# Kernel tuning notes

Measured on AMD Instinct MI355X. Metric: run time of the kernel, lower is better.

## Reference

```python
import jax, jax.numpy as jnp
import numpy as np

N = 100000   # num_nodes
E = 1000000  # num_edges
H = 64       # h_dim
OUT = 16     # out_dim (num classes)
R = 90       # num_rels
B = 8        # num_bases


def setup_inputs() -> dict:
    key = jax.random.key(0)
    ks = jax.random.split(key, 16)
    feats = jax.random.normal(ks[0], (N, H), dtype=jnp.float32)
    src = jax.random.randint(ks[1], (E,), 0, N)
    dst = jax.random.randint(ks[2], (E,), 0, N)
    etype = jax.random.randint(ks[3], (E,), 0, R)
    norm = jax.random.uniform(ks[4], (E, 1), dtype=jnp.float32)
    s_in = 1.0 / np.sqrt(H)
    s_b = 1.0 / np.sqrt(B)
    # layer 0: H->H, layer 1 (hidden): H->H, layer 2: H->OUT
    coeff0 = jax.random.normal(ks[5], (R, B), dtype=jnp.float32) * s_b
    bases0 = jax.random.normal(ks[6], (B, H, H), dtype=jnp.float32) * s_in
    bias0 = jnp.zeros((H,), dtype=jnp.float32)
    coeff1 = jax.random.normal(ks[7], (R, B), dtype=jnp.float32) * s_b
    bases1 = jax.random.normal(ks[8], (B, H, H), dtype=jnp.float32) * s_in
    bias1 = jnp.zeros((H,), dtype=jnp.float32)
    coeff2 = jax.random.normal(ks[9], (R, B), dtype=jnp.float32) * s_b
    bases2 = jax.random.normal(ks[10], (B, H, OUT), dtype=jnp.float32) * s_in
    bias2 = jnp.zeros((OUT,), dtype=jnp.float32)
    return {
        "feats": feats,
        "coeff0": coeff0, "bases0": bases0, "bias0": bias0,
        "coeff1": coeff1, "bases1": bases1, "bias1": bias1,
        "coeff2": coeff2, "bases2": bases2, "bias2": bias2,
        "src": src, "dst": dst, "etype": etype, "norm": norm,
    }


def _rgcn_layer(x, coeff, bases, bias, src, dst, etype, norm, relu):
    # Basis decomposition: W_r = sum_b coeff[r,b] * bases[b]
    # Project all nodes through every basis once: [N, B, out]
    Hn = jnp.einsum('ni,bio->nbo', x, bases)
    c = coeff[etype]  # [E, B] per-edge basis coefficients
    # Per-edge message m_e = (sum_b c_eb * Hn[src_e, b]) * norm_e,
    # accumulated over the (small, fixed) basis dim to avoid an [E,B,out] buffer.
    m = c[:, 0:1] * Hn[src, 0]
    for b in range(1, bases.shape[0]):
        m = m + c[:, b:b + 1] * Hn[src, b]
    m = m * norm
    h = jax.ops.segment_sum(m, dst, num_segments=x.shape[0]) + bias
    return jax.nn.relu(h) if relu else h


def reference(feats, coeff0, bases0, bias0, coeff1, bases1, bias1,
              coeff2, bases2, bias2, src, dst, etype, norm):
    h = _rgcn_layer(feats, coeff0, bases0, bias0, src, dst, etype, norm, relu=True)
    h = _rgcn_layer(h, coeff1, bases1, bias1, src, dst, etype, norm, relu=True)
    h = _rgcn_layer(h, coeff2, bases2, bias2, src, dst, etype, norm, relu=False)
    return h
```

## Files before the change

### kernel.cpp

```cpp
#include <hip/hip_runtime.h>
#include <hip/hip_bf16.h>
#include <cstdint>

#define NNODES 100000
#define NEDGES 1000000
#define HDIM 64
#define ODIM 16
#define NB 8
#define NREL 90
#define KDIM (HDIM * NB)

typedef short short8 __attribute__((ext_vector_type(8)));
typedef float f32x4  __attribute__((ext_vector_type(4)));
union FragU { uint4 u; short8 s; };

__device__ __forceinline__ float asf(uint32_t u) { float f; __builtin_memcpy(&f, &u, 4); return f; }
__device__ __forceinline__ uint32_t asu(float f) { uint32_t u; __builtin_memcpy(&u, &f, 4); return u; }
__device__ __forceinline__ uint16_t f2bf(float f) {
    uint32_t x = asu(f);
    return (uint16_t)((x + 0x7FFFu + ((x >> 16) & 1u)) >> 16);
}
__device__ __forceinline__ uint32_t pack2(float lo, float hi) {
    return (uint32_t)f2bf(lo) | ((uint32_t)f2bf(hi) << 16);
}
__device__ __forceinline__ void fmaC(const float4& cA, const float4& cB, float xs,
                                     float* __restrict__ acc) {
    acc[0] = fmaf(cA.x, xs, acc[0]); acc[1] = fmaf(cA.y, xs, acc[1]);
    acc[2] = fmaf(cA.z, xs, acc[2]); acc[3] = fmaf(cA.w, xs, acc[3]);
    acc[4] = fmaf(cB.x, xs, acc[4]); acc[5] = fmaf(cB.y, xs, acc[5]);
    acc[6] = fmaf(cB.z, xs, acc[6]); acc[7] = fmaf(cB.w, xs, acc[7]);
}

__global__ void cast_kernel(const float* __restrict__ in, uint16_t* __restrict__ out, int n4) {
    const int stride = (int)(gridDim.x * blockDim.x);
    for (int idx = (int)(blockIdx.x * blockDim.x + threadIdx.x); idx < n4; idx += stride) {
        float4 v = reinterpret_cast<const float4*>(in)[idx];
        uint2 p;
        p.x = pack2(v.x, v.y);
        p.y = pack2(v.z, v.w);
        reinterpret_cast<uint2*>(out)[idx] = p;
    }
}

__global__ void zero_kernel(int* __restrict__ p, int n) {
    for (int i = (int)(blockIdx.x * blockDim.x + threadIdx.x); i < n;
         i += (int)(gridDim.x * blockDim.x)) p[i] = 0;
}

__global__ void hist_kernel(const int* __restrict__ dst, int* __restrict__ cnt, int nE) {
    for (int e = (int)(blockIdx.x * blockDim.x + threadIdx.x); e < nE;
         e += (int)(gridDim.x * blockDim.x)) atomicAdd(&cnt[dst[e]], 1);
}

#define SCAN_B 512
__launch_bounds__(SCAN_B)
__global__ void scan_partial_kernel(const int* __restrict__ cnt, int* __restrict__ bsum, int n) {
    __shared__ int sh[SCAN_B];
    int id = (int)(blockIdx.x * SCAN_B + threadIdx.x);
    sh[threadIdx.x] = (id < n) ? cnt[id] : 0;
    __syncthreads();
    for (int off = SCAN_B / 2; off > 0; off >>= 1) {
        if ((int)threadIdx.x < off) sh[threadIdx.x] += sh[threadIdx.x + off];
        __syncthreads();
    }
    if (threadIdx.x == 0) bsum[blockIdx.x] = sh[0];
}

__launch_bounds__(256)
__global__ void scan_base_kernel(const int* __restrict__ bsum, int* __restrict__ bbase,
                                 int* __restrict__ offs, int nblk, int nNodes) {
    __shared__ int sh[256];
    const int t = (int)threadIdx.x;
    int v = (t < nblk) ? bsum[t] : 0;
    sh[t] = v;
    __syncthreads();
    for (int off = 1; off < 256; off <<= 1) {
        int tmp = (t >= off) ? sh[t - off] : 0;
        __syncthreads();
        sh[t] += tmp;
        __syncthreads();
    }
    if (t < nblk) bbase[t] = sh[t] - v;
    if (t == 255) offs[nNodes] = sh[255];
}

__launch_bounds__(SCAN_B)
__global__ void scan_final_kernel(int* __restrict__ cnt, const int* __restrict__ bbase,
                                  int* __restrict__ offs, int n) {
    __shared__ int sh[SCAN_B];
    int id = (int)(blockIdx.x * SCAN_B + threadIdx.x);
    int v = (id < n) ? cnt[id] : 0;
    sh[threadIdx.x] = v;
    __syncthreads();
    for (int off = 1; off < SCAN_B; off <<= 1) {
        int tmp = ((int)threadIdx.x >= off) ? sh[threadIdx.x - off] : 0;
        __syncthreads();
        sh[threadIdx.x] += tmp;
        __syncthreads();
    }
    if (id < n) {
        int excl = sh[threadIdx.x] - v + bbase[blockIdx.x];
        offs[id] = excl;
        cnt[id]  = excl;
    }
}

__global__ void scatter_kernel(const int* __restrict__ src, const int* __restrict__ dst,
                               const int* __restrict__ et, const float* __restrict__ norm,
                               int* __restrict__ cursor, uint2* __restrict__ rec, int nE) {
    const int tid    = (int)(blockIdx.x * blockDim.x + threadIdx.x);
    const int stride = (int)(gridDim.x * blockDim.x);
    int e = tid * 4;
    for (; e + 4 <= nE; e += stride * 4) {
        const int4   d4 = *reinterpret_cast<const int4*>(dst + e);
        const int4   s4 = *reinterpret_cast<const int4*>(src + e);
        const int4   t4 = *reinterpret_cast<const int4*>(et + e);
        const float4 n4 = *reinterpret_cast<const float4*>(norm + e);
        const int p0 = atomicAdd(&cursor[d4.x], 1);
        const int p1 = atomicAdd(&cursor[d4.y], 1);
        const int p2 = atomicAdd(&cursor[d4.z], 1);
        const int p3 = atomicAdd(&cursor[d4.w], 1);
        rec[p0] = make_uint2((uint32_t)s4.x | ((uint32_t)t4.x << 20), asu(n4.x));
        rec[p1] = make_uint2((uint32_t)s4.y | ((uint32_t)t4.y << 20), asu(n4.y));
        rec[p2] = make_uint2((uint32_t)s4.z | ((uint32_t)t4.z << 20), asu(n4.z));
        rec[p3] = make_uint2((uint32_t)s4.w | ((uint32_t)t4.w << 20), asu(n4.w));
    }
    for (; e < nE; e++) {
        int p = atomicAdd(&cursor[dst[e]], 1);
        rec[p] = make_uint2((uint32_t)src[e] | ((uint32_t)et[e] << 20), asu(norm[e]));
    }
}

__launch_bounds__(256)
__global__ void csr_agg_kernel(const uint16_t* __restrict__ x,
                               const float* __restrict__ coeff,
                               const int* __restrict__ offs,
                               const uint2* __restrict__ rec,
                               uint16_t* __restrict__ G, int nNodes) {
    __shared__ __align__(16) float cS[NREL * NB];
    for (int i = (int)threadIdx.x; i < NREL * NB; i += 256) cS[i] = coeff[i];
    __syncthreads();

    const int hl   = (int)threadIdx.x & 31;
    const int hwid = (int)((blockIdx.x * blockDim.x + threadIdx.x) >> 5);
    const int nhw  = (int)((gridDim.x * blockDim.x) >> 5);

    for (int d = hwid; d < nNodes; d += nhw) {
        const int j0 = offs[d], j1 = offs[d + 1];
        float accL[NB] = {0.f, 0.f, 0.f, 0.f, 0.f, 0.f, 0.f, 0.f};
        float accH[NB] = {0.f, 0.f, 0.f, 0.f, 0.f, 0.f, 0.f, 0.f};
        int j = j0;
        for (; j + 8 <= j1; j += 8) {
            uint2 r[8];
#pragma unroll
            for (int u = 0; u < 8; u++) r[u] = rec[j + u];
            uint32_t w[8];
#pragma unroll
            for (int u = 0; u < 8; u++)
                w[u] = *reinterpret_cast<const uint32_t*>(
                    x + (size_t)(r[u].x & 0xFFFFFu) * HDIM + 2 * hl);
#pragma unroll
            for (int u = 0; u < 8; u++) {
                const float4 cA = *reinterpret_cast<const float4*>(cS + (r[u].x >> 20) * NB);
                const float4 cB = *reinterpret_cast<const float4*>(cS + (r[u].x >> 20) * NB + 4);
                const float nm = asf(r[u].y);
                fmaC(cA, cB, asf(w[u] << 16) * nm, accL);
                fmaC(cA, cB, asf(w[u] & 0xFFFF0000u) * nm, accH);
            }
        }
        for (; j < j1; j++) {
            const uint2 r0 = rec[j];
            const uint32_t w0 = *reinterpret_cast<const uint32_t*>(
                x + (size_t)(r0.x & 0xFFFFFu) * HDIM + 2 * hl);
            const float4 cA = *reinterpret_cast<const float4*>(cS + (r0.x >> 20) * NB);
            const float4 cB = *reinterpret_cast<const float4*>(cS + (r0.x >> 20) * NB + 4);
            const float nm = asf(r0.y);
            fmaC(cA, cB, asf(w0 << 16) * nm, accL);
            fmaC(cA, cB, asf(w0 & 0xFFFF0000u) * nm, accH);
        }
        uint4 lo, hi;
        lo.x = pack2(accL[0], accL[1]); lo.y = pack2(accL[2], accL[3]);
        lo.z = pack2(accL[4], accL[5]); lo.w = pack2(accL[6], accL[7]);
        hi.x = pack2(accH[0], accH[1]); hi.y = pack2(accH[2], accH[3]);
        hi.z = pack2(accH[4], accH[5]); hi.w = pack2(accH[6], accH[7]);
        uint16_t* gp = G + (size_t)d * KDIM + hl * 16;
        *reinterpret_cast<uint4*>(gp)     = lo;
        *reinterpret_cast<uint4*>(gp + 8) = hi;
    }
}

__launch_bounds__(256, 3)
__global__ void proj_hidden_kernel(const uint16_t* __restrict__ G,
                                   const float* __restrict__ bases,
                                   const float* __restrict__ bias,
                                   uint16_t* __restrict__ xout, int nNodes) {
    const int t    = (int)threadIdx.x;
    const int lane = t & 63;
    const int ot   = t >> 6;
    const int q    = lane >> 4;
    const int c    = lane & 15;

    FragU bf[16];
#pragma unroll
    for (int kb = 0; kb < 16; kb++) {
#pragma unroll
        for (int j = 0; j < 8; j++) {
            const int k = kb * 32 + q * 8 + j;
            const int i = k >> 3, b = k & 7;
            bf[kb].s[j] = (short)f2bf(bases[(size_t)(b * HDIM + i) * HDIM + ot * 16 + c]);
        }
    }
    const float bv = bias[ot * 16 + c];

    const int nTiles = (nNodes + 63) / 64;
    for (int tile = (int)blockIdx.x; tile < nTiles; tile += (int)gridDim.x) {
#pragma unroll
        for (int g = 0; g < 4; g++) {
            int arow = tile * 64 + g * 16 + c;
            if (arow > nNodes - 1) arow = nNodes - 1;
            const uint16_t* gp = G + (size_t)arow * KDIM + q * 8;

            f32x4 acc = {0.f, 0.f, 0.f, 0.f};
#pragma unroll
            for (int kb = 0; kb < 16; kb++) {
                FragU a;
                a.u = *reinterpret_cast<const uint4*>(gp + kb * 32);
                acc = __builtin_amdgcn_mfma_f32_16x16x32_bf16(a.s, bf[kb].s, acc, 0, 0, 0);
            }

            const int nbase = tile * 64 + g * 16 + q * 4;
#pragma unroll
            for (int r = 0; r < 4; r++) {
                const int node = nbase + r;
                if (node < nNodes) {
                    float v = fmaxf(acc[r] + bv, 0.f);
                    xout[(size_t)node * HDIM + ot * 16 + c] = f2bf(v);
                }
            }
        }
    }
}

__launch_bounds__(256, 3)
__global__ void proj_out_kernel(const uint16_t* __restrict__ G,
                                const float* __restrict__ bases,
                                const float* __restrict__ bias,
                                float* __restrict__ out, int nNodes) {
    const int t    = (int)threadIdx.x;
    const int lane = t & 63;
    const int w    = t >> 6;
    const int q    = lane >> 4;
    const int c    = lane & 15;

    FragU bf[16];
#pragma unroll
    for (int kb = 0; kb < 16; kb++) {
#pragma unroll
        for (int j = 0; j < 8; j++) {
            const int k = kb * 32 + q * 8 + j;
            const int i = k >> 3, b = k & 7;
            bf[kb].s[j] = (short)f2bf(bases[(size_t)(b * HDIM + i) * ODIM + c]);
        }
    }
    const float bv = bias[c];

    const int nTiles = (nNodes + 63) / 64;
    for (int tile = (int)blockIdx.x; tile < nTiles; tile += (int)gridDim.x) {
        int arow = tile * 64 + w * 16 + c;
        if (arow > nNodes - 1) arow = nNodes - 1;
        const uint16_t* gp = G + (size_t)arow * KDIM + q * 8;

        f32x4 acc = {0.f, 0.f, 0.f, 0.f};
#pragma unroll
        for (int kb = 0; kb < 16; kb++) {
            FragU a;
            a.u = *reinterpret_cast<const uint4*>(gp + kb * 32);
            acc = __builtin_amdgcn_mfma_f32_16x16x32_bf16(a.s, bf[kb].s, acc, 0, 0, 0);
        }

        const int nbase = tile * 64 + w * 16 + q * 4;
#pragma unroll
        for (int r = 0; r < 4; r++) {
            const int node = nbase + r;
            if (node < nNodes) out[(size_t)node * ODIM + c] = acc[r] + bv;
        }
    }
}

extern "C" void kernel_launch(void* const* d_in, const int* in_sizes, int n_in,
                              void* d_out, int out_size, void* d_ws, size_t ws_size,
                              hipStream_t stream) {
    const float* feats  = (const float*)d_in[0];
    const float* coeff0 = (const float*)d_in[1];
    const float* bases0 = (const float*)d_in[2];
    const float* bias0  = (const float*)d_in[3];
    const float* coeff1 = (const float*)d_in[4];
    const float* bases1 = (const float*)d_in[5];
    const float* bias1  = (const float*)d_in[6];
    const float* coeff2 = (const float*)d_in[7];
    const float* bases2 = (const float*)d_in[8];
    const float* bias2  = (const float*)d_in[9];
    const int*   src    = (const int*)d_in[10];
    const int*   dst    = (const int*)d_in[11];
    const int*   etype  = (const int*)d_in[12];
    const float* norm   = (const float*)d_in[13];
    float* out = (float*)d_out;

    char* base = (char*)d_ws;
    uint16_t* G = (uint16_t*)base;
    uint16_t* x = (uint16_t*)(base + (size_t)NNODES * KDIM * 2);
    const size_t OFF_OFFS  = 115200000;
    const size_t OFF_CURS  = OFF_OFFS + 400016;
    const size_t OFF_BSUM  = OFF_CURS + 400016;
    const size_t OFF_BBASE = OFF_BSUM + 1024;
    const size_t OFF_REC   = OFF_BBASE + 1024;
    int*   offs  = (int*)(base + OFF_OFFS);
    int*   curs  = (int*)(base + OFF_CURS);
    int*   bsum  = (int*)(base + OFF_BSUM);
    int*   bbase = (int*)(base + OFF_BBASE);
    uint2* rec   = (uint2*)(base + OFF_REC);

    const int nblk = (NNODES + SCAN_B - 1) / SCAN_B;

    hipLaunchKernelGGL(zero_kernel, dim3(256), dim3(256), 0, stream, curs, NNODES);
    hipLaunchKernelGGL(hist_kernel, dim3(2048), dim3(256), 0, stream, dst, curs, NEDGES);
    hipLaunchKernelGGL(scan_partial_kernel, dim3(nblk), dim3(SCAN_B), 0, stream, curs, bsum, NNODES);
    hipLaunchKernelGGL(scan_base_kernel, dim3(1), dim3(256), 0, stream, bsum, bbase, offs, nblk, NNODES);
    hipLaunchKernelGGL(scan_final_kernel, dim3(nblk), dim3(SCAN_B), 0, stream, curs, bbase, offs, NNODES);
    hipLaunchKernelGGL(scatter_kernel, dim3(1024), dim3(256), 0, stream,
                       src, dst, etype, norm, curs, rec, NEDGES);

    hipLaunchKernelGGL(cast_kernel, dim3(2048), dim3(256), 0, stream,
                       feats, x, NNODES * HDIM / 4);

    hipLaunchKernelGGL(csr_agg_kernel, dim3(2048), dim3(256), 0, stream,
                       x, coeff0, offs, rec, G, NNODES);
    hipLaunchKernelGGL(proj_hidden_kernel, dim3(1024), dim3(256), 0, stream,
                       G, bases0, bias0, x, NNODES);
    hipLaunchKernelGGL(csr_agg_kernel, dim3(2048), dim3(256), 0, stream,
                       x, coeff1, offs, rec, G, NNODES);
    hipLaunchKernelGGL(proj_hidden_kernel, dim3(1024), dim3(256), 0, stream,
                       G, bases1, bias1, x, NNODES);
    hipLaunchKernelGGL(csr_agg_kernel, dim3(2048), dim3(256), 0, stream,
                       x, coeff2, offs, rec, G, NNODES);
    hipLaunchKernelGGL(proj_out_kernel, dim3(1024), dim3(256), 0, stream,
                       G, bases2, bias2, out, NNODES);
}
```

Before: 498.2 us.

## Pad CSR counters to cache lines and stage G tiles in LDS

The histogram and cursor counters are spread out to one per 64 bytes and placed in the start of the G workspace, so atomics on nearby destinations stop contending on shared cache lines. The scatter loop becomes a simple grid-stride loop over single edges with twice as many blocks. The hidden projection kernel now loads each 64-row G tile cooperatively into swizzled LDS with coalesced reads before the MFMA loop, replacing strided per-lane global loads. This costs more zeroing traffic, 64KB of LDS per block and lower occupancy, plus two barriers per tile.

After: 448.5 us. 10.0% less time.

```diff
diff --git a/kernel.cpp b/kernel.cpp
--- a/kernel.cpp
+++ b/kernel.cpp
@@ -9,6 +9,7 @@
 #define NB 8
 #define NREL 90
 #define KDIM (HDIM * NB)
+#define CPAD 16
 
 typedef short short8 __attribute__((ext_vector_type(8)));
 typedef float f32x4  __attribute__((ext_vector_type(4)));
@@ -49,7 +50,7 @@
 
 __global__ void hist_kernel(const int* __restrict__ dst, int* __restrict__ cnt, int nE) {
     for (int e = (int)(blockIdx.x * blockDim.x + threadIdx.x); e < nE;
-         e += (int)(gridDim.x * blockDim.x)) atomicAdd(&cnt[dst[e]], 1);
+         e += (int)(gridDim.x * blockDim.x)) atomicAdd(&cnt[dst[e] * CPAD], 1);
 }
 
 #define SCAN_B 512
@@ -57,7 +58,7 @@
 __global__ void scan_partial_kernel(const int* __restrict__ cnt, int* __restrict__ bsum, int n) {
     __shared__ int sh[SCAN_B];
     int id = (int)(blockIdx.x * SCAN_B + threadIdx.x);
-    sh[threadIdx.x] = (id < n) ? cnt[id] : 0;
+    sh[threadIdx.x] = (id < n) ? cnt[id * CPAD] : 0;
     __syncthreads();
     for (int off = SCAN_B / 2; off > 0; off >>= 1) {
         if ((int)threadIdx.x < off) sh[threadIdx.x] += sh[threadIdx.x + off];
@@ -89,7 +90,7 @@
                                   int* __restrict__ offs, int n) {
     __shared__ int sh[SCAN_B];
     int id = (int)(blockIdx.x * SCAN_B + threadIdx.x);
-    int v = (id < n) ? cnt[id] : 0;
+    int v = (id < n) ? cnt[id * CPAD] : 0;
     sh[threadIdx.x] = v;
     __syncthreads();
     for (int off = 1; off < SCAN_B; off <<= 1) {
@@ -101,32 +102,16 @@
     if (id < n) {
         int excl = sh[threadIdx.x] - v + bbase[blockIdx.x];
         offs[id] = excl;
-        cnt[id]  = excl;
+        cnt[id * CPAD] = excl;
     }
 }
 
 __global__ void scatter_kernel(const int* __restrict__ src, const int* __restrict__ dst,
                                const int* __restrict__ et, const float* __restrict__ norm,
                                int* __restrict__ cursor, uint2* __restrict__ rec, int nE) {
-    const int tid    = (int)(blockIdx.x * blockDim.x + threadIdx.x);
-    const int stride = (int)(gridDim.x * blockDim.x);
-    int e = tid * 4;
-    for (; e + 4 <= nE; e += stride * 4) {
-        const int4   d4 = *reinterpret_cast<const int4*>(dst + e);
-        const int4   s4 = *reinterpret_cast<const int4*>(src + e);
-        const int4   t4 = *reinterpret_cast<const int4*>(et + e);
-        const float4 n4 = *reinterpret_cast<const float4*>(norm + e);
-        const int p0 = atomicAdd(&cursor[d4.x], 1);
-        const int p1 = atomicAdd(&cursor[d4.y], 1);
-        const int p2 = atomicAdd(&cursor[d4.z], 1);
-        const int p3 = atomicAdd(&cursor[d4.w], 1);
-        rec[p0] = make_uint2((uint32_t)s4.x | ((uint32_t)t4.x << 20), asu(n4.x));
-        rec[p1] = make_uint2((uint32_t)s4.y | ((uint32_t)t4.y << 20), asu(n4.y));
-        rec[p2] = make_uint2((uint32_t)s4.z | ((uint32_t)t4.z << 20), asu(n4.z));
-        rec[p3] = make_uint2((uint32_t)s4.w | ((uint32_t)t4.w << 20), asu(n4.w));
-    }
-    for (; e < nE; e++) {
-        int p = atomicAdd(&cursor[dst[e]], 1);
+    for (int e = (int)(blockIdx.x * blockDim.x + threadIdx.x); e < nE;
+         e += (int)(gridDim.x * blockDim.x)) {
+        int p = atomicAdd(&cursor[dst[e] * CPAD], 1);
         rec[p] = make_uint2((uint32_t)src[e] | ((uint32_t)et[e] << 20), asu(norm[e]));
     }
 }
@@ -189,11 +174,13 @@
     }
 }
 
-__launch_bounds__(256, 3)
+__launch_bounds__(256, 2)
 __global__ void proj_hidden_kernel(const uint16_t* __restrict__ G,
                                    const float* __restrict__ bases,
                                    const float* __restrict__ bias,
                                    uint16_t* __restrict__ xout, int nNodes) {
+    __shared__ __align__(16) uint4 Gs4[64 * 64];
+
     const int t    = (int)threadIdx.x;
     const int lane = t & 63;
     const int ot   = t >> 6;
@@ -214,20 +201,25 @@
 
     const int nTiles = (nNodes + 63) / 64;
     for (int tile = (int)blockIdx.x; tile < nTiles; tile += (int)gridDim.x) {
+        for (int idx = t; idx < 64 * 64; idx += 256) {
+            const int row = idx >> 6, g = idx & 63;
+            int arow = tile * 64 + row;
+            if (arow > nNodes - 1) arow = nNodes - 1;
+            Gs4[(row << 6) | (g ^ (row & 7))] =
+                *reinterpret_cast<const uint4*>(G + (size_t)arow * KDIM + g * 8);
+        }
+        __syncthreads();
+
 #pragma unroll
         for (int g = 0; g < 4; g++) {
-            int arow = tile * 64 + g * 16 + c;
-            if (arow > nNodes - 1) arow = nNodes - 1;
-            const uint16_t* gp = G + (size_t)arow * KDIM + q * 8;
-
+            const int row = g * 16 + c;
             f32x4 acc = {0.f, 0.f, 0.f, 0.f};
 #pragma unroll
             for (int kb = 0; kb < 16; kb++) {
                 FragU a;
-                a.u = *reinterpret_cast<const uint4*>(gp + kb * 32);
+                a.u = Gs4[(row << 6) | ((kb * 4 + q) ^ (row & 7))];
                 acc = __builtin_amdgcn_mfma_f32_16x16x32_bf16(a.s, bf[kb].s, acc, 0, 0, 0);
             }
-
             const int nbase = tile * 64 + g * 16 + q * 4;
 #pragma unroll
             for (int r = 0; r < 4; r++) {
@@ -238,6 +230,7 @@
                 }
             }
         }
+        __syncthreads();
     }
 }
 
@@ -308,26 +301,25 @@
 
     char* base = (char*)d_ws;
     uint16_t* G = (uint16_t*)base;
+    int* curs   = (int*)base;
     uint16_t* x = (uint16_t*)(base + (size_t)NNODES * KDIM * 2);
     const size_t OFF_OFFS  = 115200000;
-    const size_t OFF_CURS  = OFF_OFFS + 400016;
-    const size_t OFF_BSUM  = OFF_CURS + 400016;
+    const size_t OFF_BSUM  = OFF_OFFS + 800032;
     const size_t OFF_BBASE = OFF_BSUM + 1024;
     const size_t OFF_REC   = OFF_BBASE + 1024;
     int*   offs  = (int*)(base + OFF_OFFS);
-    int*   curs  = (int*)(base + OFF_CURS);
     int*   bsum  = (int*)(base + OFF_BSUM);
     int*   bbase = (int*)(base + OFF_BBASE);
     uint2* rec   = (uint2*)(base + OFF_REC);
 
     const int nblk = (NNODES + SCAN_B - 1) / SCAN_B;
 
-    hipLaunchKernelGGL(zero_kernel, dim3(256), dim3(256), 0, stream, curs, NNODES);
+    hipLaunchKernelGGL(zero_kernel, dim3(2048), dim3(256), 0, stream, curs, NNODES * CPAD);
     hipLaunchKernelGGL(hist_kernel, dim3(2048), dim3(256), 0, stream, dst, curs, NEDGES);
     hipLaunchKernelGGL(scan_partial_kernel, dim3(nblk), dim3(SCAN_B), 0, stream, curs, bsum, NNODES);
     hipLaunchKernelGGL(scan_base_kernel, dim3(1), dim3(256), 0, stream, bsum, bbase, offs, nblk, NNODES);
     hipLaunchKernelGGL(scan_final_kernel, dim3(nblk), dim3(SCAN_B), 0, stream, curs, bbase, offs, NNODES);
-    hipLaunchKernelGGL(scatter_kernel, dim3(1024), dim3(256), 0, stream,
+    hipLaunchKernelGGL(scatter_kernel, dim3(2048), dim3(256), 0, stream,
                        src, dst, etype, norm, curs, rec, NEDGES);
 
     hipLaunchKernelGGL(cast_kernel, dim3(2048), dim3(256), 0, stream,
```
